# Kernel optimization log

Hardware: AMD Instinct MI355X
Metric: run time of the kernel (lower is better)

The kernel has to match this reference:

```python
import jax, jax.numpy as jnp
import numpy as np

B, S, D = 1, 2048, 1024
H, KVH, HD = 16, 4, 64   # D == H * HD; GQA repeat = H // KVH = 4
E, A, I = 8, 2, 3584
EPS = 1e-05
ROPE_BASE = 10000.0


def setup_inputs() -> dict:
    key = jax.random.key(0)
    ks = jax.random.split(key, 8)
    s = 0.02  # weight init scale
    x = jax.random.normal(ks[0], (B, S, D), jnp.float32)
    wqkv = jax.random.normal(ks[1], ((H + 2 * KVH) * HD, D), jnp.float32) * s
    wo = jax.random.normal(ks[2], (D, D), jnp.float32) * s
    gate_w = jax.random.normal(ks[3], (E, D), jnp.float32) * s
    w1 = jax.random.normal(ks[4], (E, I, D), jnp.float32) * s
    w2 = jax.random.normal(ks[5], (E, D, I), jnp.float32) * s
    w3 = jax.random.normal(ks[6], (E, I, D), jnp.float32) * s
    attn_norm_w = jnp.ones((D,), jnp.float32)
    ffn_norm_w = jnp.ones((D,), jnp.float32)
    # rotary table: [S, HD//2, 2] = (cos, sin)
    half = HD // 2
    inv_freq = 1.0 / (ROPE_BASE ** (np.arange(half, dtype=np.float32) / half))
    ang = np.outer(np.arange(S, dtype=np.float32), inv_freq)
    freqs_cis = jnp.asarray(np.stack([np.cos(ang), np.sin(ang)], -1), jnp.float32)
    mask = jnp.tril(jnp.ones((S, S), bool))  # causal, True = attend
    return dict(x=x, wqkv=wqkv, wo=wo, gate_w=gate_w, w1=w1, w2=w2, w3=w3,
                attn_norm_w=attn_norm_w, ffn_norm_w=ffn_norm_w,
                freqs_cis=freqs_cis, mask=mask)


def rmsnorm(x, w, eps=EPS):
    xf = x.astype(jnp.float32)
    n = xf * jax.lax.rsqrt(jnp.mean(xf * xf, axis=-1, keepdims=True) + eps)
    return n.astype(x.dtype) * w


def rope(x, freqs_cis):
    # x: [B, S, h, HD]; freqs_cis: [S, HD//2, 2]
    xs = x.reshape(*x.shape[:-1], -1, 2)
    f = freqs_cis.reshape(1, xs.shape[1], 1, xs.shape[3], 2)
    out = jnp.stack([xs[..., 0] * f[..., 0] - xs[..., 1] * f[..., 1],
                     xs[..., 1] * f[..., 0] + xs[..., 0] * f[..., 1]], axis=-1)
    return out.reshape(x.shape).astype(x.dtype)


def reference(x, wqkv, wo, gate_w, w1, w2, w3, attn_norm_w, ffn_norm_w, freqs_cis, mask):
    # ---- attention ----
    hn = rmsnorm(x, attn_norm_w)
    qkv = hn @ wqkv.T
    kv_size = KVH * HD
    q, k, v = jnp.split(qkv, [D, D + kv_size], axis=-1)
    q = rope(q.reshape(B, S, H, HD), freqs_cis).transpose(0, 2, 1, 3)    # [B,H,S,HD]
    k = rope(k.reshape(B, S, KVH, HD), freqs_cis).transpose(0, 2, 1, 3)  # [B,KVH,S,HD]
    v = v.reshape(B, S, KVH, HD).transpose(0, 2, 1, 3)
    rep = H // KVH
    k = jnp.repeat(k, rep, axis=1)
    v = jnp.repeat(v, rep, axis=1)
    scores = jnp.einsum('bhqd,bhkd->bhqk', q, k) / np.float32(np.sqrt(HD))
    scores = jnp.where(mask, scores, jnp.float32(-1e30))
    probs = jax.nn.softmax(scores, axis=-1)
    y = jnp.einsum('bhqk,bhkd->bhqd', probs, v)
    y = y.transpose(0, 2, 1, 3).reshape(B, S, D)
    h = x + y @ wo.T
    # ---- MoE FFN ----
    hf = rmsnorm(h, ffn_norm_w).reshape(-1, D)            # [T, D]
    gates = jax.nn.softmax(hf @ gate_w.T, axis=-1)        # [T, E]
    ew, ei = jax.lax.top_k(gates, A)                      # [T, A]
    ew = ew / jnp.sum(ew, axis=-1, keepdims=True)
    # math identical to gathering w1/w3/w2 per token, but computed as
    # dense all-expert GEMMs followed by an output gather (no weight replication)
    x1 = jax.nn.silu(jnp.einsum('td,eod->teo', hf, w1))   # [T, E, I]
    x3 = jnp.einsum('td,eod->teo', hf, w3)
    out_all = jnp.einsum('teo,edo->ted', x1 * x3, w2)     # [T, E, D]
    eo = jnp.take_along_axis(out_all, ei[:, :, None], axis=1)  # [T, A, D]
    ffn = jnp.einsum('tad,ta->td', eo, ew).reshape(B, S, D)
    return h + ffn
```

## Files before the change

### kernel.cpp

```cpp
#include <hip/hip_runtime.h>
#include <hip/hip_bf16.h>
#include <math.h>

#define SS 2048
#define DD 1024
#define NH 16
#define NKVH 4
#define HDIM 64
#define NE 8
#define NI 3584
#define QKVN 1536
#define PCAP 5120
#define NTILEMAX 40

typedef unsigned short u16;
typedef short short8 __attribute__((ext_vector_type(8)));
typedef float floatx4 __attribute__((ext_vector_type(4)));

__device__ inline u16 f2bf(float f) {
  unsigned u = __float_as_uint(f);
  unsigned r = u + 0x7fffu + ((u >> 16) & 1u);
  return (u16)(r >> 16);
}
__device__ inline float bf2f(u16 h) { return __uint_as_float((unsigned)h << 16); }

__global__ void f32_to_bf16_kernel(const float* __restrict__ in, u16* __restrict__ out, int n4) {
  int i = blockIdx.x * 256 + threadIdx.x;
  if (i >= n4) return;
  float4 v = ((const float4*)in)[i];
  ((ushort4*)out)[i] = make_ushort4(f2bf(v.x), f2bf(v.y), f2bf(v.z), f2bf(v.w));
}

__global__ void rmsnorm_kernel(const float* __restrict__ x, const float* __restrict__ w,
                               float* __restrict__ o32, u16* __restrict__ o16) {
  int row = blockIdx.x;
  int t = threadIdx.x;
  float4 v = ((const float4*)(x + (size_t)row * DD))[t];
  float ss = v.x * v.x + v.y * v.y + v.z * v.z + v.w * v.w;
  for (int o = 32; o > 0; o >>= 1) ss += __shfl_xor(ss, o);
  __shared__ float red[4];
  if ((t & 63) == 0) red[t >> 6] = ss;
  __syncthreads();
  float tot = red[0] + red[1] + red[2] + red[3];
  float r = rsqrtf(tot * (1.f / DD) + 1e-5f);
  float4 wv = ((const float4*)w)[t];
  float4 o;
  o.x = v.x * r * wv.x; o.y = v.y * r * wv.y; o.z = v.z * r * wv.z; o.w = v.w * r * wv.w;
  if (o32) ((float4*)(o32 + (size_t)row * DD))[t] = o;
  if (o16) ((ushort4*)(o16 + (size_t)row * DD))[t] =
      make_ushort4(f2bf(o.x), f2bf(o.y), f2bf(o.z), f2bf(o.w));
}

__global__ __launch_bounds__(256) void gemm128(
    const u16* __restrict__ A, const u16* __restrict__ B,
    float* __restrict__ C, const float* __restrict__ addend, int N, int K) {
  __shared__ u16 As[128 * 32];
  __shared__ u16 Bs[128 * 32];
  int tid = threadIdx.x;
  int bm = blockIdx.x * 128;
  int bn = blockIdx.y * 128;
  const u16* Ag = A + (size_t)bm * K;
  const u16* Bg = B + (size_t)bn * K;
  int wave = tid >> 6, lane = tid & 63;
  int wm = wave >> 1, wn = wave & 1;
  int ml = lane & 15, quad = lane >> 4;

  floatx4 acc[4][4];
#pragma unroll
  for (int i = 0; i < 4; i++)
#pragma unroll
    for (int j = 0; j < 4; j++) acc[i][j] = (floatx4){0.f, 0.f, 0.f, 0.f};

  for (int k0 = 0; k0 < K; k0 += 32) {
#pragma unroll
    for (int r = 0; r < 2; r++) {
      int s = tid + r * 256;
      int row = s >> 2, kc = (s & 3) * 8;
      __builtin_amdgcn_global_load_lds(
          (const __attribute__((address_space(1))) unsigned*)(Ag + (size_t)row * K + k0 + kc),
          (__attribute__((address_space(3))) unsigned*)(As + s * 8), 16, 0, 0);
      __builtin_amdgcn_global_load_lds(
          (const __attribute__((address_space(1))) unsigned*)(Bg + (size_t)row * K + k0 + kc),
          (__attribute__((address_space(3))) unsigned*)(Bs + s * 8), 16, 0, 0);
    }
    __syncthreads();
    short8 a[4], b[4];
#pragma unroll
    for (int i = 0; i < 4; i++)
      a[i] = *(const short8*)(As + ((wm * 64 + i * 16 + ml) * 32 + quad * 8));
#pragma unroll
    for (int j = 0; j < 4; j++)
      b[j] = *(const short8*)(Bs + ((wn * 64 + j * 16 + ml) * 32 + quad * 8));
#pragma unroll
    for (int i = 0; i < 4; i++)
#pragma unroll
      for (int j = 0; j < 4; j++)
        acc[i][j] = __builtin_amdgcn_mfma_f32_16x16x32_bf16(a[i], b[j], acc[i][j], 0, 0, 0);
    __syncthreads();
  }
#pragma unroll
  for (int i = 0; i < 4; i++) {
#pragma unroll
    for (int j = 0; j < 4; j++) {
#pragma unroll
      for (int r = 0; r < 4; r++) {
        int row = bm + wm * 64 + i * 16 + quad * 4 + r;
        int col = bn + wn * 64 + j * 16 + ml;
        size_t idx = (size_t)row * N + col;
        float v = acc[i][j][r];
        if (addend) v += addend[idx];
        C[idx] = v;
      }
    }
  }
}

__global__ __launch_bounds__(256, 3) void moe_stage1(
    const u16* __restrict__ xslot, const float* __restrict__ w1f, const float* __restrict__ w3f,
    const int* __restrict__ tmap, u16* __restrict__ x13) {
  __shared__ u16 As[128 * 32];
  __shared__ u16 B1s[64 * 32];
  __shared__ u16 B3s[64 * 32];
  int tI = blockIdx.y % NTILEMAX;
  int cI = blockIdx.x + 8 * (blockIdx.y / NTILEMAX);
  if (tI >= tmap[0]) return;
  int entry = tmap[1 + tI];
  int e = entry & 7;
  int row0 = (entry >> 3) * 128;
  int bn = cI * 64;
  const u16* Ag = xslot + (size_t)row0 * DD;
  const float* B1g = w1f + (size_t)e * NI * DD + (size_t)bn * DD;
  const float* B3g = w3f + (size_t)e * NI * DD + (size_t)bn * DD;
  int tid = threadIdx.x, wave = tid >> 6, lane = tid & 63;
  int wm = wave >> 1, wn = wave & 1;
  int ml = lane & 15, quad = lane >> 4;

  int brow = tid >> 2, bc8 = tid & 3;
  int wbyte = (brow * 64 + bc8 * 16) ^ ((brow & 6) << 3);
  const float* b1p = B1g + (size_t)brow * DD + bc8 * 8;
  const float* b3p = B3g + (size_t)brow * DD + bc8 * 8;

  floatx4 acc1[4][2], acc3[4][2];
#pragma unroll
  for (int i = 0; i < 4; i++)
#pragma unroll
    for (int j = 0; j < 2; j++) {
      acc1[i][j] = (floatx4){0.f, 0.f, 0.f, 0.f};
      acc3[i][j] = (floatx4){0.f, 0.f, 0.f, 0.f};
    }

  for (int k0 = 0; k0 < DD; k0 += 32) {
#pragma unroll
    for (int r = 0; r < 2; r++) {
      int s = tid + r * 256;
      int row = s >> 2;
      int sc = (s & 3) ^ ((row >> 1) & 3);
      __builtin_amdgcn_global_load_lds(
          (const __attribute__((address_space(1))) unsigned*)(Ag + (size_t)row * DD + k0 + sc * 8),
          (__attribute__((address_space(3))) unsigned*)(As + s * 8), 16, 0, 0);
    }
    float4 u0 = *(const float4*)(b1p + k0);
    float4 u1 = *(const float4*)(b1p + k0 + 4);
    float4 v0 = *(const float4*)(b3p + k0);
    float4 v1 = *(const float4*)(b3p + k0 + 4);
    short8 pb1, pb3;
    pb1[0] = (short)f2bf(u0.x); pb1[1] = (short)f2bf(u0.y);
    pb1[2] = (short)f2bf(u0.z); pb1[3] = (short)f2bf(u0.w);
    pb1[4] = (short)f2bf(u1.x); pb1[5] = (short)f2bf(u1.y);
    pb1[6] = (short)f2bf(u1.z); pb1[7] = (short)f2bf(u1.w);
    pb3[0] = (short)f2bf(v0.x); pb3[1] = (short)f2bf(v0.y);
    pb3[2] = (short)f2bf(v0.z); pb3[3] = (short)f2bf(v0.w);
    pb3[4] = (short)f2bf(v1.x); pb3[5] = (short)f2bf(v1.y);
    pb3[6] = (short)f2bf(v1.z); pb3[7] = (short)f2bf(v1.w);
    *(short8*)((char*)B1s + wbyte) = pb1;
    *(short8*)((char*)B3s + wbyte) = pb3;
    __syncthreads();
    short8 a[4], b1[2], b3[2];
#pragma unroll
    for (int i = 0; i < 4; i++) {
      int row = wm * 64 + i * 16 + ml;
      int rb = (row * 64 + quad * 16) ^ ((row & 6) << 3);
      a[i] = *(const short8*)((const char*)As + rb);
    }
#pragma unroll
    for (int j = 0; j < 2; j++) {
      int rr = wn * 32 + j * 16 + ml;
      int rb = (rr * 64 + quad * 16) ^ ((rr & 6) << 3);
      b1[j] = *(const short8*)((const char*)B1s + rb);
      b3[j] = *(const short8*)((const char*)B3s + rb);
    }
#pragma unroll
    for (int i = 0; i < 4; i++)
#pragma unroll
      for (int j = 0; j < 2; j++) {
        acc1[i][j] = __builtin_amdgcn_mfma_f32_16x16x32_bf16(a[i], b1[j], acc1[i][j], 0, 0, 0);
        acc3[i][j] = __builtin_amdgcn_mfma_f32_16x16x32_bf16(a[i], b3[j], acc3[i][j], 0, 0, 0);
      }
    __syncthreads();
  }
#pragma unroll
  for (int i = 0; i < 4; i++) {
#pragma unroll
    for (int j = 0; j < 2; j++) {
#pragma unroll
      for (int r = 0; r < 4; r++) {
        int row = row0 + wm * 64 + i * 16 + quad * 4 + r;
        int col = bn + wn * 32 + j * 16 + ml;
        float v1 = acc1[i][j][r], v3 = acc3[i][j][r];
        float sil = v1 / (1.f + __expf(-v1));
        x13[(size_t)row * NI + col] = f2bf(sil * v3);
      }
    }
  }
}

__global__ __launch_bounds__(256, 3) void moe_stage2(
    const u16* __restrict__ x13, const float* __restrict__ w2f,
    const int* __restrict__ tmap, float* __restrict__ pbuf) {
  __shared__ u16 As[128 * 32];
  __shared__ u16 Bs[64 * 32];
  int tI = blockIdx.y % NTILEMAX;
  int g = blockIdx.x + 8 * (blockIdx.y / NTILEMAX);
  int nt = g & 15, kh = g >> 4;
  if (tI >= tmap[0]) return;
  int entry = tmap[1 + tI];
  int e = entry & 7;
  int row0 = (entry >> 3) * 128;
  int bn = nt * 64;
  int kbeg = kh * (NI / 2), kend = kbeg + NI / 2;
  const u16* Ag = x13 + (size_t)row0 * NI;
  const float* Bg = w2f + (size_t)e * DD * NI + (size_t)bn * NI;
  float* Cp = pbuf + (size_t)kh * PCAP * DD;
  int tid = threadIdx.x, wave = tid >> 6, lane = tid & 63;
  int wm = wave >> 1, wn = wave & 1;
  int ml = lane & 15, quad = lane >> 4;

  int brow = tid >> 2, bc8 = tid & 3;
  int wbyte = (brow * 64 + bc8 * 16) ^ ((brow & 6) << 3);
  const float* bp = Bg + (size_t)brow * NI + bc8 * 8;

  floatx4 acc[4][2];
#pragma unroll
  for (int i = 0; i < 4; i++)
#pragma unroll
    for (int j = 0; j < 2; j++) acc[i][j] = (floatx4){0.f, 0.f, 0.f, 0.f};

  for (int k0 = kbeg; k0 < kend; k0 += 32) {
#pragma unroll
    for (int r = 0; r < 2; r++) {
      int s = tid + r * 256;
      int row = s >> 2;
      int sc = (s & 3) ^ ((row >> 1) & 3);
      __builtin_amdgcn_global_load_lds(
          (const __attribute__((address_space(1))) unsigned*)(Ag + (size_t)row * NI + k0 + sc * 8),
          (__attribute__((address_space(3))) unsigned*)(As + s * 8), 16, 0, 0);
    }
    float4 u0 = *(const float4*)(bp + k0);
    float4 u1 = *(const float4*)(bp + k0 + 4);
    short8 pb;
    pb[0] = (short)f2bf(u0.x); pb[1] = (short)f2bf(u0.y);
    pb[2] = (short)f2bf(u0.z); pb[3] = (short)f2bf(u0.w);
    pb[4] = (short)f2bf(u1.x); pb[5] = (short)f2bf(u1.y);
    pb[6] = (short)f2bf(u1.z); pb[7] = (short)f2bf(u1.w);
    *(short8*)((char*)Bs + wbyte) = pb;
    __syncthreads();
    short8 a[4], b[2];
#pragma unroll
    for (int i = 0; i < 4; i++) {
      int row = wm * 64 + i * 16 + ml;
      int rb = (row * 64 + quad * 16) ^ ((row & 6) << 3);
      a[i] = *(const short8*)((const char*)As + rb);
    }
#pragma unroll
    for (int j = 0; j < 2; j++) {
      int rr = wn * 32 + j * 16 + ml;
      int rb = (rr * 64 + quad * 16) ^ ((rr & 6) << 3);
      b[j] = *(const short8*)((const char*)Bs + rb);
    }
#pragma unroll
    for (int i = 0; i < 4; i++)
#pragma unroll
      for (int j = 0; j < 2; j++)
        acc[i][j] = __builtin_amdgcn_mfma_f32_16x16x32_bf16(a[i], b[j], acc[i][j], 0, 0, 0);
    __syncthreads();
  }
#pragma unroll
  for (int i = 0; i < 4; i++) {
#pragma unroll
    for (int j = 0; j < 2; j++) {
#pragma unroll
      for (int r = 0; r < 4; r++) {
        int row = row0 + wm * 64 + i * 16 + quad * 4 + r;
        int col = bn + wn * 32 + j * 16 + ml;
        Cp[(size_t)row * DD + col] = acc[i][j][r];
      }
    }
  }
}

__global__ void rope_kernel(const float* __restrict__ qkv, const float* __restrict__ freqs,
                            u16* __restrict__ qT, u16* __restrict__ kT) {
  int s = blockIdx.x;
  int tid = threadIdx.x;
#pragma unroll
  for (int r = 0; r < 2; r++) {
    int tt = r * 256 + tid;
    int hh = tt >> 5, i = tt & 31;
    const float* p = qkv + (size_t)s * QKVN + hh * 64 + 2 * i;
    float c = freqs[(s * 32 + i) * 2], sn = freqs[(s * 32 + i) * 2 + 1];
    float x0 = p[0], x1 = p[1];
    float r0 = (x0 * c - x1 * sn) * 0.125f;
    float r1 = (x1 * c + x0 * sn) * 0.125f;
    unsigned pk = (unsigned)f2bf(r0) | ((unsigned)f2bf(r1) << 16);
    *(unsigned*)(qT + ((size_t)hh * SS + s) * 64 + 2 * i) = pk;
  }
  if (tid < 128) {
    int hh = tid >> 5, i = tid & 31;
    const float* p = qkv + (size_t)s * QKVN + DD + hh * 64 + 2 * i;
    float c = freqs[(s * 32 + i) * 2], sn = freqs[(s * 32 + i) * 2 + 1];
    float x0 = p[0], x1 = p[1];
    float r0 = x0 * c - x1 * sn;
    float r1 = x1 * c + x0 * sn;
    unsigned pk = (unsigned)f2bf(r0) | ((unsigned)f2bf(r1) << 16);
    *(unsigned*)(kT + ((size_t)hh * SS + s) * 64 + 2 * i) = pk;
  }
}

__global__ void vtrans_kernel(const float* __restrict__ qkv, u16* __restrict__ vT2) {
  __shared__ u16 tile[64][65];
  int bs = blockIdx.x * 64;
  int bc = blockIdx.y * 64;
  int tid = threadIdx.x;
#pragma unroll
  for (int it = 0; it < 4; it++) {
    int idx = it * 256 + tid;
    int r = idx >> 4, c4 = idx & 15;
    float4 v = *(const float4*)(qkv + (size_t)(bs + r) * QKVN + DD + 256 + bc + c4 * 4);
    tile[r][c4 * 4 + 0] = f2bf(v.x);
    tile[r][c4 * 4 + 1] = f2bf(v.y);
    tile[r][c4 * 4 + 2] = f2bf(v.z);
    tile[r][c4 * 4 + 3] = f2bf(v.w);
  }
  __syncthreads();
#pragma unroll
  for (int it = 0; it < 4; it++) {
    int idx = it * 256 + tid;
    int cc = idx >> 4, s4 = idx & 15;
    ushort4 o = make_ushort4(tile[s4 * 4 + 0][cc], tile[s4 * 4 + 1][cc],
                             tile[s4 * 4 + 2][cc], tile[s4 * 4 + 3][cc]);
    *(ushort4*)(vT2 + (size_t)(bc + cc) * SS + bs + s4 * 4) = o;
  }
}

#define BQ 128
#define BKV 64
__global__ __launch_bounds__(256) void attn_flash(const u16* __restrict__ qT,
                                                  const u16* __restrict__ kT,
                                                  const u16* __restrict__ vT2,
                                                  u16* __restrict__ y) {
  __shared__ u16 Ks[2 * 64 * 32];
  __shared__ u16 Vs[2 * 64 * 32];
  __shared__ u16 Ps[2 * 128 * 36];
  int t = blockIdx.x;
  int h = blockIdx.y;
  int kvh = h >> 2;
  int bq = t * BQ;
  int tid = threadIdx.x, wave = tid >> 6, lane = tid & 63;
  int ml = lane & 15, quad = lane >> 4;

  short8 qf[2][2];
#pragma unroll
  for (int i = 0; i < 2; i++)
#pragma unroll
    for (int c = 0; c < 2; c++)
      qf[i][c] = *(const short8*)(qT + ((size_t)h * SS + bq + wave * 32 + i * 16 + ml) * 64 +
                                  c * 32 + quad * 8);

  float m_i[2][4], l_i[2][4];
  floatx4 o_acc[2][4];
#pragma unroll
  for (int i = 0; i < 2; i++)
#pragma unroll
    for (int r = 0; r < 4; r++) {
      m_i[i][r] = -1e30f;
      l_i[i][r] = 0.f;
      o_acc[i][r] = (floatx4){0.f, 0.f, 0.f, 0.f};
    }

  int nkv = 2 * t + 2;
  for (int kt = 0; kt < nkv; kt++) {
    int bk = kt * BKV;
    __syncthreads();
#pragma unroll
    for (int r = 0; r < 2; r++) {
      int ch = r * 256 + tid;
      int c = ch >> 8, srow = (ch >> 2) & 63, o8 = ch & 3;
      __builtin_amdgcn_global_load_lds(
          (const __attribute__((address_space(1))) unsigned*)(
              kT + ((size_t)kvh * SS + bk + srow) * 64 + c * 32 + o8 * 8),
          (__attribute__((address_space(3))) unsigned*)(Ks + ch * 8), 16, 0, 0);
      __builtin_amdgcn_global_load_lds(
          (const __attribute__((address_space(1))) unsigned*)(
              vT2 + ((size_t)kvh * 64 + srow) * SS + bk + c * 32 + o8 * 8),
          (__attribute__((address_space(3))) unsigned*)(Vs + ch * 8), 16, 0, 0);
    }
    __syncthreads();

    floatx4 s_acc[2][4];
#pragma unroll
    for (int i = 0; i < 2; i++)
#pragma unroll
      for (int j = 0; j < 4; j++) s_acc[i][j] = (floatx4){0.f, 0.f, 0.f, 0.f};
#pragma unroll
    for (int c = 0; c < 2; c++) {
#pragma unroll
      for (int jk = 0; jk < 4; jk++) {
        short8 kf = *(const short8*)(Ks + c * 2048 + (jk * 16 + ml) * 32 + quad * 8);
#pragma unroll
        for (int i = 0; i < 2; i++)
          s_acc[i][jk] = __builtin_amdgcn_mfma_f32_16x16x32_bf16(qf[i][c], kf, s_acc[i][jk], 0, 0, 0);
      }
    }
    if (bk + BKV - 1 > bq) {
#pragma unroll
      for (int i = 0; i < 2; i++)
#pragma unroll
        for (int jk = 0; jk < 4; jk++)
#pragma unroll
          for (int r = 0; r < 4; r++) {
            int row = bq + wave * 32 + i * 16 + quad * 4 + r;
            int col = bk + jk * 16 + ml;
            if (col > row) s_acc[i][jk][r] = -1e30f;
          }
    }
#pragma unroll
    for (int i = 0; i < 2; i++) {
#pragma unroll
      for (int r = 0; r < 4; r++) {
        float mx = -1e30f;
#pragma unroll
        for (int jk = 0; jk < 4; jk++) mx = fmaxf(mx, s_acc[i][jk][r]);
        for (int o = 1; o < 16; o <<= 1) mx = fmaxf(mx, __shfl_xor(mx, o));
        float mnew = fmaxf(m_i[i][r], mx);
        float alpha = __expf(m_i[i][r] - mnew);
        m_i[i][r] = mnew;
        float rs = 0.f;
#pragma unroll
        for (int jk = 0; jk < 4; jk++) {
          float p = __expf(s_acc[i][jk][r] - mnew);
          s_acc[i][jk][r] = p;
          rs += p;
        }
        for (int o = 1; o < 16; o <<= 1) rs += __shfl_xor(rs, o);
        l_i[i][r] = l_i[i][r] * alpha + rs;
#pragma unroll
        for (int jd = 0; jd < 4; jd++) o_acc[i][jd][r] *= alpha;
      }
    }
#pragma unroll
    for (int i = 0; i < 2; i++)
#pragma unroll
      for (int jk = 0; jk < 4; jk++)
#pragma unroll
        for (int r = 0; r < 4; r++) {
          int row = wave * 32 + i * 16 + quad * 4 + r;
          int col = jk * 16 + ml;
          Ps[(col >> 5) * (128 * 36) + row * 36 + (col & 31)] = f2bf(s_acc[i][jk][r]);
        }
#pragma unroll
    for (int kc = 0; kc < 2; kc++) {
      short8 pf[2];
#pragma unroll
      for (int i = 0; i < 2; i++)
        pf[i] = *(const short8*)(Ps + kc * (128 * 36) + (wave * 32 + i * 16 + ml) * 36 + quad * 8);
#pragma unroll
      for (int jd = 0; jd < 4; jd++) {
        short8 vf = *(const short8*)(Vs + kc * 2048 + (jd * 16 + ml) * 32 + quad * 8);
#pragma unroll
        for (int i = 0; i < 2; i++)
          o_acc[i][jd] = __builtin_amdgcn_mfma_f32_16x16x32_bf16(pf[i], vf, o_acc[i][jd], 0, 0, 0);
      }
    }
  }
#pragma unroll
  for (int i = 0; i < 2; i++) {
    float inv[4];
#pragma unroll
    for (int r = 0; r < 4; r++) inv[r] = 1.f / l_i[i][r];
#pragma unroll
    for (int jd = 0; jd < 4; jd++)
#pragma unroll
      for (int r = 0; r < 4; r++) {
        int row = bq + wave * 32 + i * 16 + quad * 4 + r;
        int col = h * 64 + jd * 16 + ml;
        y[(size_t)row * DD + col] = f2bf(o_acc[i][jd][r] * inv[r]);
      }
  }
}

__global__ __launch_bounds__(64) void gate_kernel(const float* __restrict__ hf,
                                                  const float* __restrict__ gw,
                                                  int* __restrict__ ei, float* __restrict__ ew,
                                                  int* __restrict__ cnt) {
  int t = blockIdx.x;
  int lane = threadIdx.x;
  const float* xr = hf + (size_t)t * DD;
  float acc[NE] = {};
  for (int c = 0; c < DD / 64; c++) {
    float xv = xr[lane + 64 * c];
#pragma unroll
    for (int e = 0; e < NE; e++) acc[e] += xv * gw[e * DD + lane + 64 * c];
  }
#pragma unroll
  for (int e = 0; e < NE; e++)
    for (int o = 32; o > 0; o >>= 1) acc[e] += __shfl_xor(acc[e], o);
  if (lane == 0) {
    float mx = acc[0];
    for (int e = 1; e < NE; e++) mx = fmaxf(mx, acc[e]);
    float p[NE], sum = 0.f;
    for (int e = 0; e < NE; e++) { p[e] = __expf(acc[e] - mx); sum += p[e]; }
    for (int e = 0; e < NE; e++) p[e] /= sum;
    int i0 = 0;
    for (int e = 1; e < NE; e++) if (p[e] > p[i0]) i0 = e;
    int i1 = (i0 == 0) ? 1 : 0;
    for (int e = 0; e < NE; e++) if (e != i0 && p[e] > p[i1]) i1 = e;
    float w0 = p[i0], w1 = p[i1], s = w0 + w1;
    ei[t * 2] = i0; ei[t * 2 + 1] = i1;
    ew[t * 2] = w0 / s; ew[t * 2 + 1] = w1 / s;
    atomicAdd(&cnt[i0], 1);
    atomicAdd(&cnt[i1], 1);
  }
}

__global__ void zero_cnt_kernel(int* cnt) {
  if (threadIdx.x < NE) cnt[threadIdx.x] = 0;
}

__global__ void prefix_kernel(const int* __restrict__ cnt, int* __restrict__ poff,
                              int* __restrict__ fill) {
  if (threadIdx.x == 0) {
    int pacc = 0;
    for (int e = 0; e < NE; e++) {
      poff[e] = pacc;
      pacc += (cnt[e] + 127) & ~127;
    }
    poff[NE] = pacc;
  }
  if (threadIdx.x < NE) fill[threadIdx.x] = 0;
}

__global__ void tilemap_kernel(const int* __restrict__ poff, int* __restrict__ tmap) {
  if (threadIdx.x == 0) {
    int n = 0;
    for (int e = 0; e < NE; e++) {
      int r0 = poff[e] >> 7, r1 = poff[e + 1] >> 7;
      for (int r = r0; r < r1; r++) tmap[1 + n++] = (r << 3) | e;
    }
    tmap[0] = n;
  }
}

__global__ void fill_kernel(const int* __restrict__ ei, const int* __restrict__ poff,
                            int* __restrict__ fill, int* __restrict__ slot_of) {
  int t = blockIdx.x * blockDim.x + threadIdx.x;
  if (t >= SS) return;
  for (int a = 0; a < 2; a++) {
    int e = ei[t * 2 + a];
    int pos = atomicAdd(&fill[e], 1);
    slot_of[t * 2 + a] = poff[e] + pos;
  }
}

__global__ void gather_kernel(const u16* __restrict__ hf16, const int* __restrict__ slot_of,
                              u16* __restrict__ xslot) {
  int t = blockIdx.x;
  uint2 v = ((const uint2*)(hf16 + (size_t)t * DD))[threadIdx.x];
  for (int a = 0; a < 2; a++) {
    int slot = slot_of[t * 2 + a];
    ((uint2*)(xslot + (size_t)slot * DD))[threadIdx.x] = v;
  }
}

__global__ void final_kernel(const float* __restrict__ h, const float* __restrict__ p0,
                             const float* __restrict__ p1, const int* __restrict__ slot_of,
                             const float* __restrict__ ew, float* __restrict__ out) {
  int t = blockIdx.x;
  int s0 = slot_of[t * 2], s1 = slot_of[t * 2 + 1];
  float w0 = ew[t * 2], w1 = ew[t * 2 + 1];
  float4 hv = ((const float4*)(h + (size_t)t * DD))[threadIdx.x];
  float4 a0 = ((const float4*)(p0 + (size_t)s0 * DD))[threadIdx.x];
  float4 a1 = ((const float4*)(p1 + (size_t)s0 * DD))[threadIdx.x];
  float4 b0 = ((const float4*)(p0 + (size_t)s1 * DD))[threadIdx.x];
  float4 b1 = ((const float4*)(p1 + (size_t)s1 * DD))[threadIdx.x];
  float4 o;
  o.x = hv.x + w0 * (a0.x + a1.x) + w1 * (b0.x + b1.x);
  o.y = hv.y + w0 * (a0.y + a1.y) + w1 * (b0.y + b1.y);
  o.z = hv.z + w0 * (a0.z + a1.z) + w1 * (b0.z + b1.z);
  o.w = hv.w + w0 * (a0.w + a1.w) + w1 * (b0.w + b1.w);
  ((float4*)(out + (size_t)t * DD))[threadIdx.x] = o;
}

extern "C" void kernel_launch(void* const* d_in, const int* in_sizes, int n_in,
                              void* d_out, int out_size, void* d_ws, size_t ws_size,
                              hipStream_t stream) {
  const float* x = (const float*)d_in[0];
  const float* wqkv = (const float*)d_in[1];
  const float* wo = (const float*)d_in[2];
  const float* gate_w = (const float*)d_in[3];
  const float* w1 = (const float*)d_in[4];
  const float* w2 = (const float*)d_in[5];
  const float* w3 = (const float*)d_in[6];
  const float* attn_norm_w = (const float*)d_in[7];
  const float* ffn_norm_w = (const float*)d_in[8];
  const float* freqs = (const float*)d_in[9];
  float* out = (float*)d_out;

  char* ws = (char*)d_ws;
  size_t off = 0;
  auto alloc = [&](size_t bytes) -> char* {
    char* p = ws + off;
    off = (off + bytes + 255) & ~(size_t)255;
    return p;
  };
  u16* hn16    = (u16*)alloc((size_t)SS * DD * 2);
  float* qkv   = (float*)alloc((size_t)SS * QKVN * 4);
  u16* y16     = (u16*)alloc((size_t)SS * DD * 2);
  float* hbuf  = (float*)alloc((size_t)SS * DD * 4);
  float* hf    = (float*)alloc((size_t)SS * DD * 4);
  u16* hf16    = (u16*)alloc((size_t)SS * DD * 2);
  u16* kT      = (u16*)alloc((size_t)NKVH * SS * HDIM * 2);
  u16* vT2     = (u16*)alloc((size_t)NKVH * HDIM * SS * 2);
  u16* wqkv16  = (u16*)alloc((size_t)QKVN * DD * 2);
  u16* wo16    = (u16*)alloc((size_t)DD * DD * 2);
  u16* xslot   = (u16*)alloc((size_t)PCAP * DD * 2);
  u16* x13     = (u16*)alloc((size_t)PCAP * NI * 2);
  float* pbuf  = (float*)alloc((size_t)2 * PCAP * DD * 4);
  int* ei      = (int*)alloc((size_t)SS * 2 * 4);
  float* ew    = (float*)alloc((size_t)SS * 2 * 4);
  int* slot_of = (int*)alloc((size_t)SS * 2 * 4);
  int* cnt     = (int*)alloc(NE * 4);
  int* poff    = (int*)alloc((NE + 1) * 4);
  int* fill    = (int*)alloc(NE * 4);
  int* tmap    = (int*)alloc((NTILEMAX + 1) * 4);
  u16* qT      = hn16;

  auto conv = [&](const float* src, u16* dst, size_t n) {
    int n4 = (int)(n / 4);
    f32_to_bf16_kernel<<<(n4 + 255) / 256, 256, 0, stream>>>(src, dst, n4);
  };

  zero_cnt_kernel<<<1, 64, 0, stream>>>(cnt);
  conv(wqkv, wqkv16, (size_t)QKVN * DD);
  conv(wo, wo16, (size_t)DD * DD);

  rmsnorm_kernel<<<SS, 256, 0, stream>>>(x, attn_norm_w, nullptr, hn16);
  gemm128<<<dim3(SS / 128, QKVN / 128), 256, 0, stream>>>(hn16, wqkv16, qkv, nullptr, QKVN, DD);
  rope_kernel<<<SS, 256, 0, stream>>>(qkv, freqs, qT, kT);
  vtrans_kernel<<<dim3(SS / 64, 4), 256, 0, stream>>>(qkv, vT2);
  attn_flash<<<dim3(SS / BQ, NH), 256, 0, stream>>>(qT, kT, vT2, y16);
  gemm128<<<dim3(SS / 128, DD / 128), 256, 0, stream>>>(y16, wo16, hbuf, x, DD, DD);

  rmsnorm_kernel<<<SS, 256, 0, stream>>>(hbuf, ffn_norm_w, hf, hf16);
  gate_kernel<<<SS, 64, 0, stream>>>(hf, gate_w, ei, ew, cnt);
  prefix_kernel<<<1, 64, 0, stream>>>(cnt, poff, fill);
  tilemap_kernel<<<1, 64, 0, stream>>>(poff, tmap);
  fill_kernel<<<(SS + 255) / 256, 256, 0, stream>>>(ei, poff, fill, slot_of);
  gather_kernel<<<SS, 256, 0, stream>>>(hf16, slot_of, xslot);
  moe_stage1<<<dim3(8, (NI / 64 / 8) * NTILEMAX), 256, 0, stream>>>(xslot, w1, w3, tmap, x13);
  moe_stage2<<<dim3(8, 4 * NTILEMAX), 256, 0, stream>>>(x13, w2, tmap, pbuf);
  final_kernel<<<SS, 256, 0, stream>>>(hbuf, pbuf, pbuf + (size_t)PCAP * DD, slot_of, ew, out);
}
```

Baseline: 762.2 us.

## Double-buffer LDS tiles in MoE GEMM stages to overlap loads with MFMA

```diff
diff --git a/kernel.cpp b/kernel.cpp
--- a/kernel.cpp
+++ b/kernel.cpp
@@ -118,9 +118,9 @@
 __global__ __launch_bounds__(256, 3) void moe_stage1(
     const u16* __restrict__ xslot, const float* __restrict__ w1f, const float* __restrict__ w3f,
     const int* __restrict__ tmap, u16* __restrict__ x13) {
-  __shared__ u16 As[128 * 32];
-  __shared__ u16 B1s[64 * 32];
-  __shared__ u16 B3s[64 * 32];
+  __shared__ u16 As[2][128 * 32];
+  __shared__ u16 B1s[2][64 * 32];
+  __shared__ u16 B3s[2][64 * 32];
   int tI = blockIdx.y % NTILEMAX;
   int cI = blockIdx.x + 8 * (blockIdx.y / NTILEMAX);
   if (tI >= tmap[0]) return;
@@ -140,6 +140,9 @@
   const float* b1p = B1g + (size_t)brow * DD + bc8 * 8;
   const float* b3p = B3g + (size_t)brow * DD + bc8 * 8;
 
+  int s0_ = tid, arow0 = s0_ >> 2, asc0 = (s0_ & 3) ^ ((arow0 >> 1) & 3);
+  int s1_ = tid + 256, arow1 = s1_ >> 2, asc1 = (s1_ & 3) ^ ((arow1 >> 1) & 3);
+
   floatx4 acc1[4][2], acc3[4][2];
 #pragma unroll
   for (int i = 0; i < 4; i++)
@@ -149,20 +152,17 @@
       acc3[i][j] = (floatx4){0.f, 0.f, 0.f, 0.f};
     }
 
-  for (int k0 = 0; k0 < DD; k0 += 32) {
-#pragma unroll
-    for (int r = 0; r < 2; r++) {
-      int s = tid + r * 256;
-      int row = s >> 2;
-      int sc = (s & 3) ^ ((row >> 1) & 3);
-      __builtin_amdgcn_global_load_lds(
-          (const __attribute__((address_space(1))) unsigned*)(Ag + (size_t)row * DD + k0 + sc * 8),
-          (__attribute__((address_space(3))) unsigned*)(As + s * 8), 16, 0, 0);
-    }
-    float4 u0 = *(const float4*)(b1p + k0);
-    float4 u1 = *(const float4*)(b1p + k0 + 4);
-    float4 v0 = *(const float4*)(b3p + k0);
-    float4 v1 = *(const float4*)(b3p + k0 + 4);
+  {
+    float4 u0 = *(const float4*)(b1p + 0);
+    float4 u1 = *(const float4*)(b1p + 4);
+    float4 v0 = *(const float4*)(b3p + 0);
+    float4 v1 = *(const float4*)(b3p + 4);
+    __builtin_amdgcn_global_load_lds(
+        (const __attribute__((address_space(1))) unsigned*)(Ag + (size_t)arow0 * DD + 0 + asc0 * 8),
+        (__attribute__((address_space(3))) unsigned*)(As[0] + s0_ * 8), 16, 0, 0);
+    __builtin_amdgcn_global_load_lds(
+        (const __attribute__((address_space(1))) unsigned*)(Ag + (size_t)arow1 * DD + 0 + asc1 * 8),
+        (__attribute__((address_space(3))) unsigned*)(As[0] + s1_ * 8), 16, 0, 0);
     short8 pb1, pb3;
     pb1[0] = (short)f2bf(u0.x); pb1[1] = (short)f2bf(u0.y);
     pb1[2] = (short)f2bf(u0.z); pb1[3] = (short)f2bf(u0.w);
@@ -172,22 +172,41 @@
     pb3[2] = (short)f2bf(v0.z); pb3[3] = (short)f2bf(v0.w);
     pb3[4] = (short)f2bf(v1.x); pb3[5] = (short)f2bf(v1.y);
     pb3[6] = (short)f2bf(v1.z); pb3[7] = (short)f2bf(v1.w);
-    *(short8*)((char*)B1s + wbyte) = pb1;
-    *(short8*)((char*)B3s + wbyte) = pb3;
-    __syncthreads();
+    *(short8*)((char*)B1s[0] + wbyte) = pb1;
+    *(short8*)((char*)B3s[0] + wbyte) = pb3;
+  }
+  __syncthreads();
+
+  for (int k = 0; k < DD / 32; k++) {
+    int cur = k & 1, nxt = cur ^ 1;
+    int kn = (k + 1) * 32;
+    bool pf = (k + 1 < DD / 32);
+    float4 u0, u1, v0, v1;
+    if (pf) {
+      u0 = *(const float4*)(b1p + kn);
+      u1 = *(const float4*)(b1p + kn + 4);
+      v0 = *(const float4*)(b3p + kn);
+      v1 = *(const float4*)(b3p + kn + 4);
+      __builtin_amdgcn_global_load_lds(
+          (const __attribute__((address_space(1))) unsigned*)(Ag + (size_t)arow0 * DD + kn + asc0 * 8),
+          (__attribute__((address_space(3))) unsigned*)(As[nxt] + s0_ * 8), 16, 0, 0);
+      __builtin_amdgcn_global_load_lds(
+          (const __attribute__((address_space(1))) unsigned*)(Ag + (size_t)arow1 * DD + kn + asc1 * 8),
+          (__attribute__((address_space(3))) unsigned*)(As[nxt] + s1_ * 8), 16, 0, 0);
+    }
     short8 a[4], b1[2], b3[2];
 #pragma unroll
     for (int i = 0; i < 4; i++) {
       int row = wm * 64 + i * 16 + ml;
       int rb = (row * 64 + quad * 16) ^ ((row & 6) << 3);
-      a[i] = *(const short8*)((const char*)As + rb);
+      a[i] = *(const short8*)((const char*)As[cur] + rb);
     }
 #pragma unroll
     for (int j = 0; j < 2; j++) {
       int rr = wn * 32 + j * 16 + ml;
       int rb = (rr * 64 + quad * 16) ^ ((rr & 6) << 3);
-      b1[j] = *(const short8*)((const char*)B1s + rb);
-      b3[j] = *(const short8*)((const char*)B3s + rb);
+      b1[j] = *(const short8*)((const char*)B1s[cur] + rb);
+      b3[j] = *(const short8*)((const char*)B3s[cur] + rb);
     }
 #pragma unroll
     for (int i = 0; i < 4; i++)
@@ -196,6 +215,19 @@
         acc1[i][j] = __builtin_amdgcn_mfma_f32_16x16x32_bf16(a[i], b1[j], acc1[i][j], 0, 0, 0);
         acc3[i][j] = __builtin_amdgcn_mfma_f32_16x16x32_bf16(a[i], b3[j], acc3[i][j], 0, 0, 0);
       }
+    if (pf) {
+      short8 pb1, pb3;
+      pb1[0] = (short)f2bf(u0.x); pb1[1] = (short)f2bf(u0.y);
+      pb1[2] = (short)f2bf(u0.z); pb1[3] = (short)f2bf(u0.w);
+      pb1[4] = (short)f2bf(u1.x); pb1[5] = (short)f2bf(u1.y);
+      pb1[6] = (short)f2bf(u1.z); pb1[7] = (short)f2bf(u1.w);
+      pb3[0] = (short)f2bf(v0.x); pb3[1] = (short)f2bf(v0.y);
+      pb3[2] = (short)f2bf(v0.z); pb3[3] = (short)f2bf(v0.w);
+      pb3[4] = (short)f2bf(v1.x); pb3[5] = (short)f2bf(v1.y);
+      pb3[6] = (short)f2bf(v1.z); pb3[7] = (short)f2bf(v1.w);
+      *(short8*)((char*)B1s[nxt] + wbyte) = pb1;
+      *(short8*)((char*)B3s[nxt] + wbyte) = pb3;
+    }
     __syncthreads();
   }
 #pragma unroll
@@ -217,8 +249,8 @@
 __global__ __launch_bounds__(256, 3) void moe_stage2(
     const u16* __restrict__ x13, const float* __restrict__ w2f,
     const int* __restrict__ tmap, float* __restrict__ pbuf) {
-  __shared__ u16 As[128 * 32];
-  __shared__ u16 Bs[64 * 32];
+  __shared__ u16 As[2][128 * 32];
+  __shared__ u16 Bs[2][64 * 32];
   int tI = blockIdx.y % NTILEMAX;
   int g = blockIdx.x + 8 * (blockIdx.y / NTILEMAX);
   int nt = g & 15, kh = g >> 4;
@@ -227,7 +259,7 @@
   int e = entry & 7;
   int row0 = (entry >> 3) * 128;
   int bn = nt * 64;
-  int kbeg = kh * (NI / 2), kend = kbeg + NI / 2;
+  int kbeg = kh * (NI / 2);
   const u16* Ag = x13 + (size_t)row0 * NI;
   const float* Bg = w2f + (size_t)e * DD * NI + (size_t)bn * NI;
   float* Cp = pbuf + (size_t)kh * PCAP * DD;
@@ -239,49 +271,75 @@
   int wbyte = (brow * 64 + bc8 * 16) ^ ((brow & 6) << 3);
   const float* bp = Bg + (size_t)brow * NI + bc8 * 8;
 
+  int s0_ = tid, arow0 = s0_ >> 2, asc0 = (s0_ & 3) ^ ((arow0 >> 1) & 3);
+  int s1_ = tid + 256, arow1 = s1_ >> 2, asc1 = (s1_ & 3) ^ ((arow1 >> 1) & 3);
+
   floatx4 acc[4][2];
 #pragma unroll
   for (int i = 0; i < 4; i++)
 #pragma unroll
     for (int j = 0; j < 2; j++) acc[i][j] = (floatx4){0.f, 0.f, 0.f, 0.f};
 
-  for (int k0 = kbeg; k0 < kend; k0 += 32) {
-#pragma unroll
-    for (int r = 0; r < 2; r++) {
-      int s = tid + r * 256;
-      int row = s >> 2;
-      int sc = (s & 3) ^ ((row >> 1) & 3);
-      __builtin_amdgcn_global_load_lds(
-          (const __attribute__((address_space(1))) unsigned*)(Ag + (size_t)row * NI + k0 + sc * 8),
-          (__attribute__((address_space(3))) unsigned*)(As + s * 8), 16, 0, 0);
-    }
-    float4 u0 = *(const float4*)(bp + k0);
-    float4 u1 = *(const float4*)(bp + k0 + 4);
+  {
+    float4 u0 = *(const float4*)(bp + kbeg);
+    float4 u1 = *(const float4*)(bp + kbeg + 4);
+    __builtin_amdgcn_global_load_lds(
+        (const __attribute__((address_space(1))) unsigned*)(Ag + (size_t)arow0 * NI + kbeg + asc0 * 8),
+        (__attribute__((address_space(3))) unsigned*)(As[0] + s0_ * 8), 16, 0, 0);
+    __builtin_amdgcn_global_load_lds(
+        (const __attribute__((address_space(1))) unsigned*)(Ag + (size_t)arow1 * NI + kbeg + asc1 * 8),
+        (__attribute__((address_space(3))) unsigned*)(As[0] + s1_ * 8), 16, 0, 0);
     short8 pb;
     pb[0] = (short)f2bf(u0.x); pb[1] = (short)f2bf(u0.y);
     pb[2] = (short)f2bf(u0.z); pb[3] = (short)f2bf(u0.w);
     pb[4] = (short)f2bf(u1.x); pb[5] = (short)f2bf(u1.y);
     pb[6] = (short)f2bf(u1.z); pb[7] = (short)f2bf(u1.w);
-    *(short8*)((char*)Bs + wbyte) = pb;
-    __syncthreads();
+    *(short8*)((char*)Bs[0] + wbyte) = pb;
+  }
+  __syncthreads();
+
+  const int NK = (NI / 2) / 32;
+  for (int kk = 0; kk < NK; kk++) {
+    int cur = kk & 1, nxt = cur ^ 1;
+    int kn = kbeg + (kk + 1) * 32;
+    bool pf = (kk + 1 < NK);
+    float4 u0, u1;
+    if (pf) {
+      u0 = *(const float4*)(bp + kn);
+      u1 = *(const float4*)(bp + kn + 4);
+      __builtin_amdgcn_global_load_lds(
+          (const __attribute__((address_space(1))) unsigned*)(Ag + (size_t)arow0 * NI + kn + asc0 * 8),
+          (__attribute__((address_space(3))) unsigned*)(As[nxt] + s0_ * 8), 16, 0, 0);
+      __builtin_amdgcn_global_load_lds(
+          (const __attribute__((address_space(1))) unsigned*)(Ag + (size_t)arow1 * NI + kn + asc1 * 8),
+          (__attribute__((address_space(3))) unsigned*)(As[nxt] + s1_ * 8), 16, 0, 0);
+    }
     short8 a[4], b[2];
 #pragma unroll
     for (int i = 0; i < 4; i++) {
       int row = wm * 64 + i * 16 + ml;
       int rb = (row * 64 + quad * 16) ^ ((row & 6) << 3);
-      a[i] = *(const short8*)((const char*)As + rb);
+      a[i] = *(const short8*)((const char*)As[cur] + rb);
     }
 #pragma unroll
     for (int j = 0; j < 2; j++) {
       int rr = wn * 32 + j * 16 + ml;
       int rb = (rr * 64 + quad * 16) ^ ((rr & 6) << 3);
-      b[j] = *(const short8*)((const char*)Bs + rb);
+      b[j] = *(const short8*)((const char*)Bs[cur] + rb);
     }
 #pragma unroll
     for (int i = 0; i < 4; i++)
 #pragma unroll
       for (int j = 0; j < 2; j++)
         acc[i][j] = __builtin_amdgcn_mfma_f32_16x16x32_bf16(a[i], b[j], acc[i][j], 0, 0, 0);
+    if (pf) {
+      short8 pb;
+      pb[0] = (short)f2bf(u0.x); pb[1] = (short)f2bf(u0.y);
+      pb[2] = (short)f2bf(u0.z); pb[3] = (short)f2bf(u0.w);
+      pb[4] = (short)f2bf(u1.x); pb[5] = (short)f2bf(u1.y);
+      pb[6] = (short)f2bf(u1.z); pb[7] = (short)f2bf(u1.w);
+      *(short8*)((char*)Bs[nxt] + wbyte) = pb;
+    }
     __syncthreads();
   }
 #pragma unroll
```

Result: faster. 739.3 us (-3.0%).
